# Optimization experiments

Measured on AMD Instinct MI355X. Metric: run time of the kernel, lower is better.

Reference implementation:

```python
import jax, jax.numpy as jnp
import numpy as np

B, N, D = 1, 4096, 4096  # code requires B*D == N (see norm2 broadcast)
EPS = 1e-7
NEG = -1e9


def setup_inputs() -> dict:
    key = jax.random.key(0)
    k1, k2, k3 = jax.random.split(key, 3)
    x = jax.random.normal(k1, (B, N, D), dtype=jnp.float32)
    adj = (jax.random.uniform(k2, (B, N, N)) < 0.01).astype(jnp.float32)
    eye = jnp.eye(N, dtype=jnp.float32)[None]
    adj = jnp.maximum(adj, eye)
    beta = jax.random.uniform(k3, (1,), dtype=jnp.float32)  # Parameter ~ U(0,1)
    return {"x": x, "adj": adj, "beta": beta}


def reference(x, adj, beta):
    # torch.norm(x, 2, 1): L2 norm over dim 1 (node dim) -> [B, D]; view(-1,1) -> [B*D, 1]
    norm2 = jnp.linalg.norm(x, axis=1).reshape(-1, 1)  # [B*D, 1] == [N, 1]
    denom = norm2 @ norm2.T + EPS                      # [N, N]
    # cosine-style score: beta * (x @ x^T) / denom  -> [B, N, N]
    cos = beta * jnp.matmul(x, jnp.swapaxes(x, 1, 2)) / denom
    mask = (1.0 - adj) * NEG
    P = jax.nn.softmax(cos + mask, axis=2)             # [B, N, N]
    return jnp.matmul(P, x)                            # [B, N, D]
```

## Files before the change

### kernel.cpp

```cpp
#include <hip/hip_runtime.h>
#include <stdint.h>

#define NN 4096
#define EPSV 1e-7f
#define SLABC 512
#define NSLAB (NN / SLABC)

typedef short shortx4 __attribute__((ext_vector_type(4)));
typedef float floatx2 __attribute__((ext_vector_type(2)));
typedef float floatx4 __attribute__((ext_vector_type(4)));
typedef unsigned int uintx4 __attribute__((ext_vector_type(4)));
typedef _Float16 half2t __attribute__((ext_vector_type(2)));

static __device__ __forceinline__ short f2h(float f) {
    union { _Float16 h; short s; } c;
    c.h = (_Float16)f;
    return c.s;
}

static __device__ __forceinline__ float dot2acc(unsigned a, unsigned b, float d) {
    union { unsigned u; half2t h; } ua, ub;
    ua.u = a; ub.u = b;
    d = fmaf((float)ua.h[0], (float)ub.h[0], d);
    return fmaf((float)ua.h[1], (float)ub.h[1], d);
}

__global__ __launch_bounds__(256) void fuse_cast(const float* __restrict__ x,
                                                 short* __restrict__ xh,
                                                 float* __restrict__ nsq) {
    __shared__ floatx4 cs[4][64];
    const int tx = threadIdx.x;
    const int ty = threadIdx.y;
    const int cb = blockIdx.x * 256;
    const int rb = blockIdx.y * 64;
    const int col = cb + tx * 4;
    floatx4 ss = {0.f, 0.f, 0.f, 0.f};
#pragma unroll
    for (int i = 0; i < 16; ++i) {
        const int r = rb + ty + i * 4;
        floatx4 v = __builtin_nontemporal_load((const floatx4*)(x + (size_t)r * NN + col));
        ss += v * v;
        shortx4 o;
        o[0] = f2h(v[0]); o[1] = f2h(v[1]); o[2] = f2h(v[2]); o[3] = f2h(v[3]);
        *(shortx4*)(xh + (size_t)r * NN + col) = o;
    }
    cs[ty][tx] = ss;
    __syncthreads();
    if (ty == 0) {
        floatx4 s4 = cs[0][tx] + cs[1][tx] + cs[2][tx] + cs[3][tx];
        float* np = nsq + col;
        atomicAdd(np + 0, s4[0]);
        atomicAdd(np + 1, s4[1]);
        atomicAdd(np + 2, s4[2]);
        atomicAdd(np + 3, s4[3]);
    }
}

__global__ __launch_bounds__(256) void build_idx(const float* __restrict__ adj,
                                                 unsigned short* __restrict__ idx,
                                                 int* __restrict__ cnt) {
    __shared__ int wtot[4];
    const int t = threadIdx.x;
    const int lane = t & 63;
    const int w = t >> 6;
    const size_t i = blockIdx.x;
    const floatx4* ar = (const floatx4*)(adj + i * NN) + 4 * t;
    floatx4 a0 = __builtin_nontemporal_load(ar + 0);
    floatx4 a1 = __builtin_nontemporal_load(ar + 1);
    floatx4 a2 = __builtin_nontemporal_load(ar + 2);
    floatx4 a3 = __builtin_nontemporal_load(ar + 3);
    unsigned mask = 0;
#pragma unroll
    for (int u = 0; u < 4; ++u) {
        floatx4 a = (u == 0) ? a0 : (u == 1) ? a1 : (u == 2) ? a2 : a3;
#pragma unroll
        for (int e = 0; e < 4; ++e)
            if (a[e] != 0.f) mask |= 1u << (4 * u + e);
    }
    const int h = __popc(mask);
    int sc = h;
#pragma unroll
    for (int o = 1; o < 64; o <<= 1) {
        int v = __shfl_up(sc, o, 64);
        if (lane >= o) sc += v;
    }
    if (lane == 63) wtot[w] = sc;
    __syncthreads();
    int base = 0;
#pragma unroll
    for (int ww = 0; ww < 4; ++ww)
        if (ww < w) base += wtot[ww];
    int c = wtot[0] + wtot[1] + wtot[2] + wtot[3];
    if (c > 256) c = 256;
    if (t == 0) cnt[i] = c;
    int off = base + sc - h;
    unsigned m = mask;
    while (m) {
        int b = __ffs(m) - 1;
        m &= m - 1;
        if (off < 256) idx[i * 256 + off] = (unsigned short)(16 * t + b);
        ++off;
    }
}

__global__ __launch_bounds__(256) void score_slab(const short* __restrict__ xh,
                                                  const unsigned short* __restrict__ idx,
                                                  const int* __restrict__ cnt,
                                                  float* __restrict__ score) {
    const int t = threadIdx.x;
    const int lane = t & 63;
    const int w = t >> 6;
    const int g = lane >> 3;
    const int sl = lane & 7;
    const int col0 = blockIdx.x * SLABC;
    const size_t i = (size_t)blockIdx.y * 4 + w;
    const int c = cnt[i];
    const unsigned short* irow = idx + i * 256;

    const uintx4* xr = (const uintx4*)(xh + i * NN + col0);
    uintx4 xi[8];
#pragma unroll
    for (int it = 0; it < 8; ++it) xi[it] = xr[it * 8 + sl];

    for (int r = 0; r * 8 < c; ++r) {
        const int k = r * 8 + g;
        const bool ok = k < c;
        const int kk = ok ? k : c - 1;
        const int j = irow[kk];
        const uintx4* rp = (const uintx4*)(xh + (size_t)j * NN + col0);
        uintx4 v0 = rp[0 * 8 + sl], v1 = rp[1 * 8 + sl];
        uintx4 v2 = rp[2 * 8 + sl], v3 = rp[3 * 8 + sl];
        uintx4 v4 = rp[4 * 8 + sl], v5 = rp[5 * 8 + sl];
        uintx4 v6 = rp[6 * 8 + sl], v7 = rp[7 * 8 + sl];
        float d0 = 0.f, d1 = 0.f;
#pragma unroll
        for (int u = 0; u < 4; ++u) {
            d0 = dot2acc(v0[u], xi[0][u], d0);
            d1 = dot2acc(v1[u], xi[1][u], d1);
            d0 = dot2acc(v2[u], xi[2][u], d0);
            d1 = dot2acc(v3[u], xi[3][u], d1);
            d0 = dot2acc(v4[u], xi[4][u], d0);
            d1 = dot2acc(v5[u], xi[5][u], d1);
            d0 = dot2acc(v6[u], xi[6][u], d0);
            d1 = dot2acc(v7[u], xi[7][u], d1);
        }
        float d = d0 + d1;
        d += __shfl_xor(d, 1, 64);
        d += __shfl_xor(d, 2, 64);
        d += __shfl_xor(d, 4, 64);
        if (ok && sl == 0) atomicAdd(&score[i * 256 + k], d);
    }
}

__global__ __launch_bounds__(256) void pv_slab(const short* __restrict__ xh,
                                               const float* __restrict__ nsq,
                                               const unsigned short* __restrict__ idx,
                                               const int* __restrict__ cnt,
                                               const float* __restrict__ score,
                                               const float* __restrict__ betaPtr,
                                               float* __restrict__ out) {
    __shared__ float svs[4][256];
    __shared__ unsigned short jds[4][256];
    const int t = threadIdx.x;
    const int lane = t & 63;
    const int w = t >> 6;
    const int col0 = blockIdx.x * SLABC;
    const size_t i = (size_t)blockIdx.y * 4 + w;
    const int c = cnt[i];
    const float beta = *betaPtr;
    const float ni = sqrtf(nsq[i]);

    float sreg[4];
    int jreg[4];
#pragma unroll
    for (int q = 0; q < 4; ++q) {
        const int k = lane + 64 * q;
        if (k < c) {
            const int j = idx[i * 256 + k];
            jreg[q] = j;
            sreg[q] = beta * score[i * 256 + k] / (ni * sqrtf(nsq[j]) + EPSV);
        } else {
            jreg[q] = 0;
            sreg[q] = -3.0e38f;
        }
    }
    float mx = fmaxf(fmaxf(sreg[0], sreg[1]), fmaxf(sreg[2], sreg[3]));
#pragma unroll
    for (int off = 32; off; off >>= 1) mx = fmaxf(mx, __shfl_xor(mx, off, 64));
    float sm = 0.f;
#pragma unroll
    for (int q = 0; q < 4; ++q) {
        const int k = lane + 64 * q;
        float e = (k < c) ? __expf(sreg[q] - mx) : 0.f;
        sreg[q] = e;
        sm += e;
    }
#pragma unroll
    for (int off = 32; off; off >>= 1) sm += __shfl_xor(sm, off, 64);
    const float inv = 1.f / sm;
#pragma unroll
    for (int q = 0; q < 4; ++q) {
        const int k = lane + 64 * q;
        svs[w][k] = sreg[q] * inv;
        jds[w][k] = (unsigned short)jreg[q];
    }
    __syncthreads();

    float acc[8];
#pragma unroll
    for (int e = 0; e < 8; ++e) acc[e] = 0.f;
    const short* xcol = xh + col0 + lane * 8;
    int k = 0;
    for (; k + 4 <= c; k += 4) {
        const int j0 = jds[w][k], j1 = jds[w][k + 1];
        const int j2 = jds[w][k + 2], j3 = jds[w][k + 3];
        const float p0 = svs[w][k], p1 = svs[w][k + 1];
        const float p2 = svs[w][k + 2], p3 = svs[w][k + 3];
        uintx4 v0 = *(const uintx4*)(xcol + (size_t)j0 * NN);
        uintx4 v1 = *(const uintx4*)(xcol + (size_t)j1 * NN);
        uintx4 v2 = *(const uintx4*)(xcol + (size_t)j2 * NN);
        uintx4 v3 = *(const uintx4*)(xcol + (size_t)j3 * NN);
#pragma unroll
        for (int u = 0; u < 4; ++u) {
            union { unsigned x; half2t h; } c0, c1, c2, c3;
            c0.x = v0[u]; c1.x = v1[u]; c2.x = v2[u]; c3.x = v3[u];
            float a0 = acc[2 * u], a1 = acc[2 * u + 1];
            a0 = fmaf(p0, (float)c0.h[0], a0); a1 = fmaf(p0, (float)c0.h[1], a1);
            a0 = fmaf(p1, (float)c1.h[0], a0); a1 = fmaf(p1, (float)c1.h[1], a1);
            a0 = fmaf(p2, (float)c2.h[0], a0); a1 = fmaf(p2, (float)c2.h[1], a1);
            a0 = fmaf(p3, (float)c3.h[0], a0); a1 = fmaf(p3, (float)c3.h[1], a1);
            acc[2 * u] = a0; acc[2 * u + 1] = a1;
        }
    }
    for (; k < c; ++k) {
        const int j = jds[w][k];
        const float p = svs[w][k];
        uintx4 v = *(const uintx4*)(xcol + (size_t)j * NN);
#pragma unroll
        for (int u = 0; u < 4; ++u) {
            union { unsigned x; half2t h; } cc;
            cc.x = v[u];
            acc[2 * u] = fmaf(p, (float)cc.h[0], acc[2 * u]);
            acc[2 * u + 1] = fmaf(p, (float)cc.h[1], acc[2 * u + 1]);
        }
    }
    floatx4* op = (floatx4*)(out + i * NN + col0 + lane * 8);
    floatx4 o0 = {acc[0], acc[1], acc[2], acc[3]};
    floatx4 o1 = {acc[4], acc[5], acc[6], acc[7]};
    __builtin_nontemporal_store(o0, op + 0);
    __builtin_nontemporal_store(o1, op + 1);
}

extern "C" void kernel_launch(void* const* d_in, const int* in_sizes, int n_in,
                              void* d_out, int out_size, void* d_ws, size_t ws_size,
                              hipStream_t stream) {
    const float* x = (const float*)d_in[0];
    const float* adj = (const float*)d_in[1];
    const float* beta = (const float*)d_in[2];

    const size_t XH = (size_t)32 * 1024 * 1024;
    const size_t IX = (size_t)2 * 1024 * 1024;
    const size_t SC = (size_t)4 * 1024 * 1024;
    const size_t need = XH + IX + SC + 2 * NN * sizeof(float);
    if (ws_size < need) return;

    char* ws = (char*)d_ws;
    short* xh = (short*)ws;
    unsigned short* idx = (unsigned short*)(ws + XH);
    float* score = (float*)(ws + XH + IX);
    float* nsq = (float*)(ws + XH + IX + SC);
    int* cnt = (int*)(ws + XH + IX + SC + NN * sizeof(float));

    (void)hipMemsetAsync(nsq, 0, NN * sizeof(float), stream);
    (void)hipMemsetAsync(score, 0, SC, stream);
    fuse_cast<<<dim3(16, 64), dim3(64, 4), 0, stream>>>(x, xh, nsq);
    build_idx<<<NN, 256, 0, stream>>>(adj, idx, cnt);
    score_slab<<<dim3(NSLAB, NN / 4), 256, 0, stream>>>(xh, idx, cnt, score);
    pv_slab<<<dim3(NSLAB, NN / 4), 256, 0, stream>>>(xh, nsq, idx, cnt, score, beta, (float*)d_out);
}
```

Measured before the change: 310.1 us.

## Merge prep kernels and software-pipeline gathers in score and PV kernels

Combines the fp16 cast/norm kernel and the adjacency index-building kernel into one launch, with block ranges selecting the role, so both memory-bound passes run concurrently and one launch is dropped. In score_slab and pv_slab, the next group of gathered rows is loaded before the current group is computed (register double-buffering). This hides gather latency. score_slab also uses four accumulators instead of two to shorten the dependency chain. The cost is higher register pressure, which may reduce occupancy, and a few redundant clamped loads at the tail.

```diff
diff --git a/kernel.cpp b/kernel.cpp
--- a/kernel.cpp
+++ b/kernel.cpp
@@ -25,81 +25,82 @@
     return fmaf((float)ua.h[1], (float)ub.h[1], d);
 }
 
-__global__ __launch_bounds__(256) void fuse_cast(const float* __restrict__ x,
-                                                 short* __restrict__ xh,
-                                                 float* __restrict__ nsq) {
+__global__ __launch_bounds__(256) void prep(const float* __restrict__ x,
+                                            const float* __restrict__ adj,
+                                            short* __restrict__ xh,
+                                            float* __restrict__ nsq,
+                                            unsigned short* __restrict__ idx,
+                                            int* __restrict__ cnt) {
     __shared__ floatx4 cs[4][64];
-    const int tx = threadIdx.x;
-    const int ty = threadIdx.y;
-    const int cb = blockIdx.x * 256;
-    const int rb = blockIdx.y * 64;
-    const int col = cb + tx * 4;
-    floatx4 ss = {0.f, 0.f, 0.f, 0.f};
-#pragma unroll
-    for (int i = 0; i < 16; ++i) {
-        const int r = rb + ty + i * 4;
-        floatx4 v = __builtin_nontemporal_load((const floatx4*)(x + (size_t)r * NN + col));
-        ss += v * v;
-        shortx4 o;
-        o[0] = f2h(v[0]); o[1] = f2h(v[1]); o[2] = f2h(v[2]); o[3] = f2h(v[3]);
-        *(shortx4*)(xh + (size_t)r * NN + col) = o;
-    }
-    cs[ty][tx] = ss;
-    __syncthreads();
-    if (ty == 0) {
-        floatx4 s4 = cs[0][tx] + cs[1][tx] + cs[2][tx] + cs[3][tx];
-        float* np = nsq + col;
-        atomicAdd(np + 0, s4[0]);
-        atomicAdd(np + 1, s4[1]);
-        atomicAdd(np + 2, s4[2]);
-        atomicAdd(np + 3, s4[3]);
-    }
-}
-
-__global__ __launch_bounds__(256) void build_idx(const float* __restrict__ adj,
-                                                 unsigned short* __restrict__ idx,
-                                                 int* __restrict__ cnt) {
     __shared__ int wtot[4];
+    const int bid = blockIdx.x;
     const int t = threadIdx.x;
     const int lane = t & 63;
     const int w = t >> 6;
-    const size_t i = blockIdx.x;
-    const floatx4* ar = (const floatx4*)(adj + i * NN) + 4 * t;
-    floatx4 a0 = __builtin_nontemporal_load(ar + 0);
-    floatx4 a1 = __builtin_nontemporal_load(ar + 1);
-    floatx4 a2 = __builtin_nontemporal_load(ar + 2);
-    floatx4 a3 = __builtin_nontemporal_load(ar + 3);
-    unsigned mask = 0;
-#pragma unroll
-    for (int u = 0; u < 4; ++u) {
-        floatx4 a = (u == 0) ? a0 : (u == 1) ? a1 : (u == 2) ? a2 : a3;
-#pragma unroll
-        for (int e = 0; e < 4; ++e)
-            if (a[e] != 0.f) mask |= 1u << (4 * u + e);
-    }
-    const int h = __popc(mask);
-    int sc = h;
-#pragma unroll
-    for (int o = 1; o < 64; o <<= 1) {
-        int v = __shfl_up(sc, o, 64);
-        if (lane >= o) sc += v;
-    }
-    if (lane == 63) wtot[w] = sc;
-    __syncthreads();
-    int base = 0;
-#pragma unroll
-    for (int ww = 0; ww < 4; ++ww)
-        if (ww < w) base += wtot[ww];
-    int c = wtot[0] + wtot[1] + wtot[2] + wtot[3];
-    if (c > 256) c = 256;
-    if (t == 0) cnt[i] = c;
-    int off = base + sc - h;
-    unsigned m = mask;
-    while (m) {
-        int b = __ffs(m) - 1;
-        m &= m - 1;
-        if (off < 256) idx[i * 256 + off] = (unsigned short)(16 * t + b);
-        ++off;
+
+    if (bid < 1024) {
+        const int cb = (bid & 15) * 256;
+        const int rb = (bid >> 4) * 64;
+        const int col = cb + lane * 4;
+        floatx4 ss = {0.f, 0.f, 0.f, 0.f};
+#pragma unroll
+        for (int i = 0; i < 16; ++i) {
+            const int r = rb + w + i * 4;
+            floatx4 v = __builtin_nontemporal_load((const floatx4*)(x + (size_t)r * NN + col));
+            ss += v * v;
+            shortx4 o;
+            o[0] = f2h(v[0]); o[1] = f2h(v[1]); o[2] = f2h(v[2]); o[3] = f2h(v[3]);
+            *(shortx4*)(xh + (size_t)r * NN + col) = o;
+        }
+        cs[w][lane] = ss;
+        __syncthreads();
+        if (w == 0) {
+            floatx4 s4 = cs[0][lane] + cs[1][lane] + cs[2][lane] + cs[3][lane];
+            float* np = nsq + col;
+            atomicAdd(np + 0, s4[0]);
+            atomicAdd(np + 1, s4[1]);
+            atomicAdd(np + 2, s4[2]);
+            atomicAdd(np + 3, s4[3]);
+        }
+    } else {
+        const size_t i = (size_t)(bid - 1024);
+        const floatx4* ar = (const floatx4*)(adj + i * NN) + 4 * t;
+        floatx4 a0 = __builtin_nontemporal_load(ar + 0);
+        floatx4 a1 = __builtin_nontemporal_load(ar + 1);
+        floatx4 a2 = __builtin_nontemporal_load(ar + 2);
+        floatx4 a3 = __builtin_nontemporal_load(ar + 3);
+        unsigned mask = 0;
+#pragma unroll
+        for (int u = 0; u < 4; ++u) {
+            floatx4 a = (u == 0) ? a0 : (u == 1) ? a1 : (u == 2) ? a2 : a3;
+#pragma unroll
+            for (int e = 0; e < 4; ++e)
+                if (a[e] != 0.f) mask |= 1u << (4 * u + e);
+        }
+        const int h = __popc(mask);
+        int sc = h;
+#pragma unroll
+        for (int o = 1; o < 64; o <<= 1) {
+            int v = __shfl_up(sc, o, 64);
+            if (lane >= o) sc += v;
+        }
+        if (lane == 63) wtot[w] = sc;
+        __syncthreads();
+        int base = 0;
+#pragma unroll
+        for (int ww = 0; ww < 4; ++ww)
+            if (ww < w) base += wtot[ww];
+        int c = wtot[0] + wtot[1] + wtot[2] + wtot[3];
+        if (c > 256) c = 256;
+        if (t == 0) cnt[i] = c;
+        int off = base + sc - h;
+        unsigned m = mask;
+        while (m) {
+            int b = __ffs(m) - 1;
+            m &= m - 1;
+            if (off < 256) idx[i * 256 + off] = (unsigned short)(16 * t + b);
+            ++off;
+        }
     }
 }
 
@@ -122,33 +123,40 @@
 #pragma unroll
     for (int it = 0; it < 8; ++it) xi[it] = xr[it * 8 + sl];
 
-    for (int r = 0; r * 8 < c; ++r) {
-        const int k = r * 8 + g;
-        const bool ok = k < c;
-        const int kk = ok ? k : c - 1;
-        const int j = irow[kk];
-        const uintx4* rp = (const uintx4*)(xh + (size_t)j * NN + col0);
-        uintx4 v0 = rp[0 * 8 + sl], v1 = rp[1 * 8 + sl];
-        uintx4 v2 = rp[2 * 8 + sl], v3 = rp[3 * 8 + sl];
-        uintx4 v4 = rp[4 * 8 + sl], v5 = rp[5 * 8 + sl];
-        uintx4 v6 = rp[6 * 8 + sl], v7 = rp[7 * 8 + sl];
-        float d0 = 0.f, d1 = 0.f;
+    const int nr = (c + 7) >> 3;
+    const int kf = g < c ? g : c - 1;
+    const uintx4* rp = (const uintx4*)(xh + (size_t)irow[kf] * NN + col0);
+    uintx4 V0 = rp[sl],      V1 = rp[8 + sl],  V2 = rp[16 + sl], V3 = rp[24 + sl];
+    uintx4 V4 = rp[32 + sl], V5 = rp[40 + sl], V6 = rp[48 + sl], V7 = rp[56 + sl];
+
+    for (int r = 0; r < nr; ++r) {
+        const int kn = (r + 1) * 8 + g;
+        const int kc = kn < c ? kn : c - 1;
+        const uintx4* rn = (const uintx4*)(xh + (size_t)irow[kc] * NN + col0);
+        uintx4 W0 = rn[sl],      W1 = rn[8 + sl],  W2 = rn[16 + sl], W3 = rn[24 + sl];
+        uintx4 W4 = rn[32 + sl], W5 = rn[40 + sl], W6 = rn[48 + sl], W7 = rn[56 + sl];
+
+        float d0 = 0.f, d1 = 0.f, d2 = 0.f, d3 = 0.f;
 #pragma unroll
         for (int u = 0; u < 4; ++u) {
-            d0 = dot2acc(v0[u], xi[0][u], d0);
-            d1 = dot2acc(v1[u], xi[1][u], d1);
-            d0 = dot2acc(v2[u], xi[2][u], d0);
-            d1 = dot2acc(v3[u], xi[3][u], d1);
-            d0 = dot2acc(v4[u], xi[4][u], d0);
-            d1 = dot2acc(v5[u], xi[5][u], d1);
-            d0 = dot2acc(v6[u], xi[6][u], d0);
-            d1 = dot2acc(v7[u], xi[7][u], d1);
-        }
-        float d = d0 + d1;
+            d0 = dot2acc(V0[u], xi[0][u], d0);
+            d1 = dot2acc(V1[u], xi[1][u], d1);
+            d2 = dot2acc(V2[u], xi[2][u], d2);
+            d3 = dot2acc(V3[u], xi[3][u], d3);
+            d0 = dot2acc(V4[u], xi[4][u], d0);
+            d1 = dot2acc(V5[u], xi[5][u], d1);
+            d2 = dot2acc(V6[u], xi[6][u], d2);
+            d3 = dot2acc(V7[u], xi[7][u], d3);
+        }
+        float d = (d0 + d1) + (d2 + d3);
         d += __shfl_xor(d, 1, 64);
         d += __shfl_xor(d, 2, 64);
         d += __shfl_xor(d, 4, 64);
-        if (ok && sl == 0) atomicAdd(&score[i * 256 + k], d);
+        const int k = r * 8 + g;
+        if (k < c && sl == 0) atomicAdd(&score[i * 256 + k], d);
+
+        V0 = W0; V1 = W1; V2 = W2; V3 = W3;
+        V4 = W4; V5 = W5; V6 = W6; V7 = W7;
     }
 }
 
@@ -206,20 +214,28 @@
     }
     __syncthreads();
 
+    const short* xcol = xh + col0 + lane * 8;
+    auto jof = [&](int kk) -> int { return jds[w][kk < c ? kk : c - 1]; };
+    auto pof = [&](int kk) -> float { return kk < c ? svs[w][kk] : 0.f; };
+
     float acc[8];
 #pragma unroll
     for (int e = 0; e < 8; ++e) acc[e] = 0.f;
-    const short* xcol = xh + col0 + lane * 8;
-    int k = 0;
-    for (; k + 4 <= c; k += 4) {
-        const int j0 = jds[w][k], j1 = jds[w][k + 1];
-        const int j2 = jds[w][k + 2], j3 = jds[w][k + 3];
-        const float p0 = svs[w][k], p1 = svs[w][k + 1];
-        const float p2 = svs[w][k + 2], p3 = svs[w][k + 3];
-        uintx4 v0 = *(const uintx4*)(xcol + (size_t)j0 * NN);
-        uintx4 v1 = *(const uintx4*)(xcol + (size_t)j1 * NN);
-        uintx4 v2 = *(const uintx4*)(xcol + (size_t)j2 * NN);
-        uintx4 v3 = *(const uintx4*)(xcol + (size_t)j3 * NN);
+
+    int j0 = jof(0), j1 = jof(1), j2 = jof(2), j3 = jof(3);
+    uintx4 v0 = *(const uintx4*)(xcol + (size_t)j0 * NN);
+    uintx4 v1 = *(const uintx4*)(xcol + (size_t)j1 * NN);
+    uintx4 v2 = *(const uintx4*)(xcol + (size_t)j2 * NN);
+    uintx4 v3 = *(const uintx4*)(xcol + (size_t)j3 * NN);
+
+    for (int k = 0; k < c; k += 4) {
+        const int n0 = jof(k + 4), n1 = jof(k + 5), n2 = jof(k + 6), n3 = jof(k + 7);
+        uintx4 w0 = *(const uintx4*)(xcol + (size_t)n0 * NN);
+        uintx4 w1 = *(const uintx4*)(xcol + (size_t)n1 * NN);
+        uintx4 w2 = *(const uintx4*)(xcol + (size_t)n2 * NN);
+        uintx4 w3 = *(const uintx4*)(xcol + (size_t)n3 * NN);
+
+        const float p0 = pof(k), p1 = pof(k + 1), p2 = pof(k + 2), p3 = pof(k + 3);
 #pragma unroll
         for (int u = 0; u < 4; ++u) {
             union { unsigned x; half2t h; } c0, c1, c2, c3;
@@ -231,19 +247,9 @@
             a0 = fmaf(p3, (float)c3.h[0], a0); a1 = fmaf(p3, (float)c3.h[1], a1);
             acc[2 * u] = a0; acc[2 * u + 1] = a1;
         }
-    }
-    for (; k < c; ++k) {
-        const int j = jds[w][k];
-        const float p = svs[w][k];
-        uintx4 v = *(const uintx4*)(xcol + (size_t)j * NN);
-#pragma unroll
-        for (int u = 0; u < 4; ++u) {
-            union { unsigned x; half2t h; } cc;
-            cc.x = v[u];
-            acc[2 * u] = fmaf(p, (float)cc.h[0], acc[2 * u]);
-            acc[2 * u + 1] = fmaf(p, (float)cc.h[1], acc[2 * u + 1]);
-        }
-    }
+        v0 = w0; v1 = w1; v2 = w2; v3 = w3;
+    }
+
     floatx4* op = (floatx4*)(out + i * NN + col0 + lane * 8);
     floatx4 o0 = {acc[0], acc[1], acc[2], acc[3]};
     floatx4 o1 = {acc[4], acc[5], acc[6], acc[7]};
@@ -273,8 +279,7 @@
 
     (void)hipMemsetAsync(nsq, 0, NN * sizeof(float), stream);
     (void)hipMemsetAsync(score, 0, SC, stream);
-    fuse_cast<<<dim3(16, 64), dim3(64, 4), 0, stream>>>(x, xh, nsq);
-    build_idx<<<NN, 256, 0, stream>>>(adj, idx, cnt);
+    prep<<<1024 + NN, 256, 0, stream>>>(x, adj, xh, nsq, idx, cnt);
     score_slab<<<dim3(NSLAB, NN / 4), 256, 0, stream>>>(xh, idx, cnt, score);
     pv_slab<<<dim3(NSLAB, NN / 4), 256, 0, stream>>>(xh, nsq, idx, cnt, score, beta, (float*)d_out);
 }
```

Measured after the change: 330.1 us. +6.5%, slower.

## Fuse prep kernels and gather neighbor rows as FP8 in score pass

Applied to the files above, without the earlier changes.

Merges the cast/norm kernel and the adjacency index builder into a single prep launch, split across block ranges. Prep also writes an FP8 copy of x when the workspace is large enough, and the score pass then gathers neighbor rows as FP8 dotted against the f16 query row. This halves the gathered bytes per neighbor. FP8 quantization of the neighbor rows reduces score precision, which the softmax amplifies through beta. The f16 fallback path now uses four accumulators instead of two.

```diff
diff --git a/kernel.cpp b/kernel.cpp
--- a/kernel.cpp
+++ b/kernel.cpp
@@ -25,88 +25,107 @@
     return fmaf((float)ua.h[1], (float)ub.h[1], d);
 }
 
-__global__ __launch_bounds__(256) void fuse_cast(const float* __restrict__ x,
-                                                 short* __restrict__ xh,
-                                                 float* __restrict__ nsq) {
+static __device__ __forceinline__ float fp8dot4(unsigned v, unsigned h0, unsigned h1, float d) {
+    floatx2 lo = __builtin_amdgcn_cvt_pk_f32_fp8(v, false);
+    floatx2 hi = __builtin_amdgcn_cvt_pk_f32_fp8(v, true);
+    union { unsigned u; half2t h; } a, b;
+    a.u = h0; b.u = h1;
+    d = fmaf(lo[0], (float)a.h[0], d);
+    d = fmaf(lo[1], (float)a.h[1], d);
+    d = fmaf(hi[0], (float)b.h[0], d);
+    return fmaf(hi[1], (float)b.h[1], d);
+}
+
+__global__ __launch_bounds__(256) void prep(const float* __restrict__ x,
+                                            const float* __restrict__ adj,
+                                            short* __restrict__ xh,
+                                            unsigned char* __restrict__ xf8,
+                                            float* __restrict__ nsq,
+                                            unsigned short* __restrict__ idx,
+                                            int* __restrict__ cnt) {
     __shared__ floatx4 cs[4][64];
-    const int tx = threadIdx.x;
-    const int ty = threadIdx.y;
-    const int cb = blockIdx.x * 256;
-    const int rb = blockIdx.y * 64;
-    const int col = cb + tx * 4;
-    floatx4 ss = {0.f, 0.f, 0.f, 0.f};
-#pragma unroll
-    for (int i = 0; i < 16; ++i) {
-        const int r = rb + ty + i * 4;
-        floatx4 v = __builtin_nontemporal_load((const floatx4*)(x + (size_t)r * NN + col));
-        ss += v * v;
-        shortx4 o;
-        o[0] = f2h(v[0]); o[1] = f2h(v[1]); o[2] = f2h(v[2]); o[3] = f2h(v[3]);
-        *(shortx4*)(xh + (size_t)r * NN + col) = o;
-    }
-    cs[ty][tx] = ss;
-    __syncthreads();
-    if (ty == 0) {
-        floatx4 s4 = cs[0][tx] + cs[1][tx] + cs[2][tx] + cs[3][tx];
-        float* np = nsq + col;
-        atomicAdd(np + 0, s4[0]);
-        atomicAdd(np + 1, s4[1]);
-        atomicAdd(np + 2, s4[2]);
-        atomicAdd(np + 3, s4[3]);
-    }
-}
-
-__global__ __launch_bounds__(256) void build_idx(const float* __restrict__ adj,
-                                                 unsigned short* __restrict__ idx,
-                                                 int* __restrict__ cnt) {
     __shared__ int wtot[4];
+    const int bid = blockIdx.x;
     const int t = threadIdx.x;
     const int lane = t & 63;
     const int w = t >> 6;
-    const size_t i = blockIdx.x;
-    const floatx4* ar = (const floatx4*)(adj + i * NN) + 4 * t;
-    floatx4 a0 = __builtin_nontemporal_load(ar + 0);
-    floatx4 a1 = __builtin_nontemporal_load(ar + 1);
-    floatx4 a2 = __builtin_nontemporal_load(ar + 2);
-    floatx4 a3 = __builtin_nontemporal_load(ar + 3);
-    unsigned mask = 0;
-#pragma unroll
-    for (int u = 0; u < 4; ++u) {
-        floatx4 a = (u == 0) ? a0 : (u == 1) ? a1 : (u == 2) ? a2 : a3;
-#pragma unroll
-        for (int e = 0; e < 4; ++e)
-            if (a[e] != 0.f) mask |= 1u << (4 * u + e);
-    }
-    const int h = __popc(mask);
-    int sc = h;
-#pragma unroll
-    for (int o = 1; o < 64; o <<= 1) {
-        int v = __shfl_up(sc, o, 64);
-        if (lane >= o) sc += v;
-    }
-    if (lane == 63) wtot[w] = sc;
-    __syncthreads();
-    int base = 0;
-#pragma unroll
-    for (int ww = 0; ww < 4; ++ww)
-        if (ww < w) base += wtot[ww];
-    int c = wtot[0] + wtot[1] + wtot[2] + wtot[3];
-    if (c > 256) c = 256;
-    if (t == 0) cnt[i] = c;
-    int off = base + sc - h;
-    unsigned m = mask;
-    while (m) {
-        int b = __ffs(m) - 1;
-        m &= m - 1;
-        if (off < 256) idx[i * 256 + off] = (unsigned short)(16 * t + b);
-        ++off;
-    }
-}
-
-__global__ __launch_bounds__(256) void score_slab(const short* __restrict__ xh,
-                                                  const unsigned short* __restrict__ idx,
-                                                  const int* __restrict__ cnt,
-                                                  float* __restrict__ score) {
+
+    if (bid < 1024) {
+        const int cb = (bid & 15) * 256;
+        const int rb = (bid >> 4) * 64;
+        const int col = cb + lane * 4;
+        floatx4 ss = {0.f, 0.f, 0.f, 0.f};
+#pragma unroll
+        for (int i = 0; i < 16; ++i) {
+            const int r = rb + w + i * 4;
+            floatx4 v = __builtin_nontemporal_load((const floatx4*)(x + (size_t)r * NN + col));
+            ss += v * v;
+            shortx4 o;
+            o[0] = f2h(v[0]); o[1] = f2h(v[1]); o[2] = f2h(v[2]); o[3] = f2h(v[3]);
+            *(shortx4*)(xh + (size_t)r * NN + col) = o;
+            if (xf8) {
+                int p = __builtin_amdgcn_cvt_pk_fp8_f32(v[0], v[1], 0, false);
+                p = __builtin_amdgcn_cvt_pk_fp8_f32(v[2], v[3], p, true);
+                *(int*)(xf8 + (size_t)r * NN + col) = p;
+            }
+        }
+        cs[w][lane] = ss;
+        __syncthreads();
+        if (w == 0) {
+            floatx4 s4 = cs[0][lane] + cs[1][lane] + cs[2][lane] + cs[3][lane];
+            float* np = nsq + col;
+            atomicAdd(np + 0, s4[0]);
+            atomicAdd(np + 1, s4[1]);
+            atomicAdd(np + 2, s4[2]);
+            atomicAdd(np + 3, s4[3]);
+        }
+    } else {
+        const size_t i = (size_t)(bid - 1024);
+        const floatx4* ar = (const floatx4*)(adj + i * NN) + 4 * t;
+        floatx4 a0 = __builtin_nontemporal_load(ar + 0);
+        floatx4 a1 = __builtin_nontemporal_load(ar + 1);
+        floatx4 a2 = __builtin_nontemporal_load(ar + 2);
+        floatx4 a3 = __builtin_nontemporal_load(ar + 3);
+        unsigned mask = 0;
+#pragma unroll
+        for (int u = 0; u < 4; ++u) {
+            floatx4 a = (u == 0) ? a0 : (u == 1) ? a1 : (u == 2) ? a2 : a3;
+#pragma unroll
+            for (int e = 0; e < 4; ++e)
+                if (a[e] != 0.f) mask |= 1u << (4 * u + e);
+        }
+        const int h = __popc(mask);
+        int sc = h;
+#pragma unroll
+        for (int o = 1; o < 64; o <<= 1) {
+            int v = __shfl_up(sc, o, 64);
+            if (lane >= o) sc += v;
+        }
+        if (lane == 63) wtot[w] = sc;
+        __syncthreads();
+        int base = 0;
+#pragma unroll
+        for (int ww = 0; ww < 4; ++ww)
+            if (ww < w) base += wtot[ww];
+        int c = wtot[0] + wtot[1] + wtot[2] + wtot[3];
+        if (c > 256) c = 256;
+        if (t == 0) cnt[i] = c;
+        int off = base + sc - h;
+        unsigned m = mask;
+        while (m) {
+            int b = __ffs(m) - 1;
+            m &= m - 1;
+            if (off < 256) idx[i * 256 + off] = (unsigned short)(16 * t + b);
+            ++off;
+        }
+    }
+}
+
+__global__ __launch_bounds__(256) void score_slab_fp8(const unsigned char* __restrict__ x8,
+                                                      const short* __restrict__ xh,
+                                                      const unsigned short* __restrict__ idx,
+                                                      const int* __restrict__ cnt,
+                                                      float* __restrict__ score) {
     const int t = threadIdx.x;
     const int lane = t & 63;
     const int w = t >> 6;
@@ -118,6 +137,60 @@
     const unsigned short* irow = idx + i * 256;
 
     const uintx4* xr = (const uintx4*)(xh + i * NN + col0);
+    uintx4 xiA[4], xiB[4];
+#pragma unroll
+    for (int it = 0; it < 4; ++it) {
+        const int m = it * 8 + sl;
+        xiA[it] = xr[2 * m];
+        xiB[it] = xr[2 * m + 1];
+    }
+
+    for (int r = 0; r * 8 < c; ++r) {
+        const int k = r * 8 + g;
+        const bool ok = k < c;
+        const int kk = ok ? k : c - 1;
+        const int j = irow[kk];
+        const uintx4* rp = (const uintx4*)(x8 + (size_t)j * NN + col0);
+        uintx4 v0 = rp[sl], v1 = rp[8 + sl], v2 = rp[16 + sl], v3 = rp[24 + sl];
+        float d0 = 0.f, d1 = 0.f, d2 = 0.f, d3 = 0.f;
+#pragma unroll
+        for (int q = 0; q < 4; ++q) {
+            const unsigned hA0 = (q < 2) ? xiA[0][2 * q] : xiB[0][2 * (q - 2)];
+            const unsigned hA1 = (q < 2) ? xiA[0][2 * q + 1] : xiB[0][2 * (q - 2) + 1];
+            d0 = fp8dot4(v0[q], hA0, hA1, d0);
+            const unsigned hB0 = (q < 2) ? xiA[1][2 * q] : xiB[1][2 * (q - 2)];
+            const unsigned hB1 = (q < 2) ? xiA[1][2 * q + 1] : xiB[1][2 * (q - 2) + 1];
+            d1 = fp8dot4(v1[q], hB0, hB1, d1);
+            const unsigned hC0 = (q < 2) ? xiA[2][2 * q] : xiB[2][2 * (q - 2)];
+            const unsigned hC1 = (q < 2) ? xiA[2][2 * q + 1] : xiB[2][2 * (q - 2) + 1];
+            d2 = fp8dot4(v2[q], hC0, hC1, d2);
+            const unsigned hD0 = (q < 2) ? xiA[3][2 * q] : xiB[3][2 * (q - 2)];
+            const unsigned hD1 = (q < 2) ? xiA[3][2 * q + 1] : xiB[3][2 * (q - 2) + 1];
+            d3 = fp8dot4(v3[q], hD0, hD1, d3);
+        }
+        float d = (d0 + d1) + (d2 + d3);
+        d += __shfl_xor(d, 1, 64);
+        d += __shfl_xor(d, 2, 64);
+        d += __shfl_xor(d, 4, 64);
+        if (ok && sl == 0) atomicAdd(&score[i * 256 + k], d);
+    }
+}
+
+__global__ __launch_bounds__(256) void score_slab_f16(const short* __restrict__ xh,
+                                                      const unsigned short* __restrict__ idx,
+                                                      const int* __restrict__ cnt,
+                                                      float* __restrict__ score) {
+    const int t = threadIdx.x;
+    const int lane = t & 63;
+    const int w = t >> 6;
+    const int g = lane >> 3;
+    const int sl = lane & 7;
+    const int col0 = blockIdx.x * SLABC;
+    const size_t i = (size_t)blockIdx.y * 4 + w;
+    const int c = cnt[i];
+    const unsigned short* irow = idx + i * 256;
+
+    const uintx4* xr = (const uintx4*)(xh + i * NN + col0);
     uintx4 xi[8];
 #pragma unroll
     for (int it = 0; it < 8; ++it) xi[it] = xr[it * 8 + sl];
@@ -128,23 +201,21 @@
         const int kk = ok ? k : c - 1;
         const int j = irow[kk];
         const uintx4* rp = (const uintx4*)(xh + (size_t)j * NN + col0);
-        uintx4 v0 = rp[0 * 8 + sl], v1 = rp[1 * 8 + sl];
-        uintx4 v2 = rp[2 * 8 + sl], v3 = rp[3 * 8 + sl];
-        uintx4 v4 = rp[4 * 8 + sl], v5 = rp[5 * 8 + sl];
-        uintx4 v6 = rp[6 * 8 + sl], v7 = rp[7 * 8 + sl];
-        float d0 = 0.f, d1 = 0.f;
+        uintx4 v0 = rp[sl], v1 = rp[8 + sl], v2 = rp[16 + sl], v3 = rp[24 + sl];
+        uintx4 v4 = rp[32 + sl], v5 = rp[40 + sl], v6 = rp[48 + sl], v7 = rp[56 + sl];
+        float d0 = 0.f, d1 = 0.f, d2 = 0.f, d3 = 0.f;
 #pragma unroll
         for (int u = 0; u < 4; ++u) {
             d0 = dot2acc(v0[u], xi[0][u], d0);
             d1 = dot2acc(v1[u], xi[1][u], d1);
-            d0 = dot2acc(v2[u], xi[2][u], d0);
-            d1 = dot2acc(v3[u], xi[3][u], d1);
+            d2 = dot2acc(v2[u], xi[2][u], d2);
+            d3 = dot2acc(v3[u], xi[3][u], d3);
             d0 = dot2acc(v4[u], xi[4][u], d0);
             d1 = dot2acc(v5[u], xi[5][u], d1);
-            d0 = dot2acc(v6[u], xi[6][u], d0);
-            d1 = dot2acc(v7[u], xi[7][u], d1);
-        }
-        float d = d0 + d1;
+            d2 = dot2acc(v6[u], xi[6][u], d2);
+            d3 = dot2acc(v7[u], xi[7][u], d3);
+        }
+        float d = (d0 + d1) + (d2 + d3);
         d += __shfl_xor(d, 1, 64);
         d += __shfl_xor(d, 2, 64);
         d += __shfl_xor(d, 4, 64);
@@ -261,8 +332,10 @@
     const size_t XH = (size_t)32 * 1024 * 1024;
     const size_t IX = (size_t)2 * 1024 * 1024;
     const size_t SC = (size_t)4 * 1024 * 1024;
-    const size_t need = XH + IX + SC + 2 * NN * sizeof(float);
-    if (ws_size < need) return;
+    const size_t XF8 = (size_t)16 * 1024 * 1024;
+    const size_t base = XH + IX + SC + 2 * NN * sizeof(float);
+    if (ws_size < base) return;
+    const bool use_fp8 = ws_size >= base + XF8;
 
     char* ws = (char*)d_ws;
     short* xh = (short*)ws;
@@ -270,11 +343,14 @@
     float* score = (float*)(ws + XH + IX);
     float* nsq = (float*)(ws + XH + IX + SC);
     int* cnt = (int*)(ws + XH + IX + SC + NN * sizeof(float));
+    unsigned char* xf8 = use_fp8 ? (unsigned char*)(ws + base) : nullptr;
 
     (void)hipMemsetAsync(nsq, 0, NN * sizeof(float), stream);
     (void)hipMemsetAsync(score, 0, SC, stream);
-    fuse_cast<<<dim3(16, 64), dim3(64, 4), 0, stream>>>(x, xh, nsq);
-    build_idx<<<NN, 256, 0, stream>>>(adj, idx, cnt);
-    score_slab<<<dim3(NSLAB, NN / 4), 256, 0, stream>>>(xh, idx, cnt, score);
+    prep<<<1024 + NN, 256, 0, stream>>>(x, adj, xh, xf8, nsq, idx, cnt);
+    if (use_fp8)
+        score_slab_fp8<<<dim3(NSLAB, NN / 4), 256, 0, stream>>>(xf8, xh, idx, cnt, score);
+    else
+        score_slab_f16<<<dim3(NSLAB, NN / 4), 256, 0, stream>>>(xh, idx, cnt, score);
     pv_slab<<<dim3(NSLAB, NN / 4), 256, 0, stream>>>(xh, nsq, idx, cnt, score, beta, (float*)d_out);
 }
```

Result: faster. 299.1 us (-3.6%).
